# Kernel optimization log

Hardware: AMD Instinct MI355X
Metric: run time of the kernel (lower is better)

## Reference

```python
import jax, jax.numpy as jnp
import numpy as np

N = 100000       # patches per slide (bag size)
D = 512          # size[1] for size_arg='big'
D_ATTN = 256     # size[2]
C = 4            # n_classes
N_REFS = 3
TP_RATE = 0.01
NP_RATE = 0.01
REF_RATE = 0.01
EPS = 1e-10


def setup_inputs() -> dict:
    key = jax.random.key(0)
    ks = jax.random.split(key, 8)
    w = lambda k, shape: jax.random.normal(k, shape, jnp.float32) * 0.02
    return {
        "h": jax.random.normal(ks[0], (N, D), jnp.float32),
        "label": jax.random.randint(ks[1], (2,), 0, C),
        "Wa": w(ks[2], (D, D_ATTN)), "ba": jnp.zeros((D_ATTN,), jnp.float32),
        "Wb": w(ks[3], (D, D_ATTN)), "bb": jnp.zeros((D_ATTN,), jnp.float32),
        "Wc": w(ks[4], (D_ATTN, C)), "bc": jnp.zeros((C,), jnp.float32),
        "Wcls": w(ks[5], (D, C)), "bcls": jnp.zeros((C,), jnp.float32),
        "Wr": w(ks[6], (N_REFS, D, C + 1)),
        "br": jnp.zeros((N_REFS, C + 1), jnp.float32),
    }


def _ce(logits, targets):
    # cross entropy with integer targets, reduction='none'
    logp = jax.nn.log_softmax(logits, axis=-1)
    return -jnp.take_along_axis(logp, targets[..., None], axis=-1)[..., 0]


def _find_candidate_loss(final_score, h, in_label, Wr, br):
    n = final_score.shape[0]
    k = max(1, int(n * TP_RATE))
    mn = final_score.min(axis=0)
    mx = final_score.max(axis=0)
    norm = (final_score - mn) / (mx - mn)                     # [N, C]
    vals, idx = jax.lax.top_k(norm.T, k)                      # [C, k]
    valid = (vals > 0.5) & in_label[:, None]                  # only classes in label
    logits = jnp.einsum('ckd,de->cke', h[idx], Wr) + br       # [C, k, C+1]
    tgt = jnp.broadcast_to(jnp.arange(C)[:, None], (C, k))
    ce_tp = _ce(logits, tgt)
    mean_score = final_score.mean(axis=1)
    k_np = int(n * NP_RATE)
    nvals, nidx = jax.lax.top_k(-mean_score, k_np)
    np_valid = (-nvals) < 0.5
    np_logits = h[nidx] @ Wr + br                             # [k_np, C+1]
    ce_np = -jax.nn.log_softmax(np_logits, axis=-1)[:, C]
    num = jnp.sum(ce_tp * valid) + jnp.sum(ce_np * np_valid)
    den = valid.sum() + np_valid.sum()
    return num / jnp.maximum(den, 1)


def _find_candidate_ref_loss(ref_score, h, in_label, Wr, br):
    n = ref_score.shape[0]
    k = max(1, int(n * REF_RATE))
    vals, idx = jax.lax.top_k(ref_score.T, k)                 # [C+1, k]
    include = jnp.concatenate([in_label, jnp.array([True])])  # bg class always included
    valid = (vals > 0.5) & include[:, None]
    logits = jnp.einsum('ckd,de->cke', h[idx], Wr) + br       # [C+1, k, C+1]
    tgt = jnp.broadcast_to(jnp.arange(C + 1)[:, None], (C + 1, k))
    ce = _ce(logits, tgt)
    return jnp.sum(ce * valid) / jnp.maximum(valid.sum(), 1)


def _forward(h, label, Wa, ba, Wb, bb, Wc, bc, Wcls, bcls, Wr, br):
    # gated attention (Attn_Net_Gated), eval mode (dropout off)
    a = jnp.tanh(h @ Wa + ba)
    b = jax.nn.sigmoid(h @ Wb + bb)
    det_logit = (a * b) @ Wc + bc                             # [N, C]
    cls_score = jax.nn.softmax(h @ Wcls + bcls, axis=1)
    det_score = jax.nn.softmax(det_logit, axis=0)             # softmax over instances
    final_score = cls_score * det_score
    in_label = jnp.any(jnp.arange(C)[:, None] == label[None, :], axis=1)  # [C] bool
    instance_loss = jnp.float32(0.0)
    ref_score = final_score
    for r in range(N_REFS):
        if r == 0:
            instance_loss = instance_loss + _find_candidate_loss(final_score, h, in_label, Wr[r], br[r])
        else:
            instance_loss = instance_loss + _find_candidate_ref_loss(ref_score, h, in_label, Wr[r], br[r])
        ref_score = jax.nn.softmax(h @ Wr[r] + br[r], axis=1)  # [N, C+1]
    Y_prob = jnp.clip(jnp.sum(final_score, axis=0), EPS, 1.0 - EPS)
    return final_score, Y_prob, ref_score, instance_loss


def reference(h, label, Wa, ba, Wb, bb, Wc, bc, Wcls, bcls, Wr, br):
    final_score, Y_prob, ref_score, instance_loss = _forward(
        h, label, Wa, ba, Wb, bb, Wc, bc, Wcls, bcls, Wr, br)
    Y_hat = jnp.argmax(Y_prob)[None]
    return final_score, Y_prob, Y_hat, ref_score, instance_loss
```

## Files before the change

kernel.cpp:

```cpp
#include <hip/hip_runtime.h>
#include <math.h>

#define NI    100000
#define KSEL  1000
#define NCOL2 640
#define HBINS 2048

#define OUT_FS   0
#define OUT_YP   400000
#define OUT_YH   400004
#define OUT_REF  400005
#define OUT_LOSS 900005

#define OFF_DET    0
#define OFF_CLS    400000
#define OFF_REF0   800000
#define OFF_REF1   1300000
#define OFF_MEAN   1800000
#define OFF_WPT    1900000
#define OFF_BPACK  2063840
#define OFF_SCAL   2064480
#define OFF_SELIDX 2064608
#define OFF_HIST   2079608

#define SC_SUMEXP 0
#define SC_YPROB  4
#define SC_FSMIN  8
#define SC_FSMAX  12
#define SC_THR    16
#define SC_INCL   20
#define SC_NUM    25
#define SC_CNT    28
#define SC_PREFIX 43
#define SC_RESTK  58

typedef short short8 __attribute__((ext_vector_type(8)));
typedef float f32x4 __attribute__((ext_vector_type(4)));

__device__ __forceinline__ unsigned fenc(float x) {
    unsigned u = __float_as_uint(x);
    return (u & 0x80000000u) ? ~u : (u | 0x80000000u);
}
__device__ __forceinline__ unsigned short f2bf(float f) {
    unsigned u = __float_as_uint(f);
    return (unsigned short)((u + 0x7FFFu + ((u >> 16) & 1u)) >> 16);
}

__global__ __launch_bounds__(256) void prep_kernel(
    const float* __restrict__ Wa, const float* __restrict__ Wb,
    const float* __restrict__ Wcls, const float* __restrict__ Wr,
    const float* __restrict__ ba, const float* __restrict__ bb,
    const float* __restrict__ bcls, const float* __restrict__ br,
    float* __restrict__ ws)
{
    const int tid0 = blockIdx.x * 256 + threadIdx.x;
    unsigned short* wpT = (unsigned short*)(ws + OFF_WPT);
    if (tid0 < NCOL2 * 512) {
        const int c = tid0 >> 9, k = tid0 & 511;
        float v = 0.f;
        if (c < 512)      { const int j = c >> 1; v = (c & 1) ? Wb[k*256 + j] : Wa[k*256 + j]; }
        else if (c < 516)   v = Wcls[k*4 + (c - 512)];
        else if (c < 531) { const int q = c - 516; v = Wr[((q/5)*512 + k)*5 + (q%5)]; }
        wpT[tid0] = f2bf(v);
    }
    if (tid0 < NCOL2) {
        float v = 0.f; const int c = tid0;
        if (c < 512)      v = (c & 1) ? bb[c >> 1] : ba[c >> 1];
        else if (c < 516) v = bcls[c - 512];
        else if (c < 531) v = br[c - 516];
        ws[OFF_BPACK + c] = v;
    }
    if (tid0 < 128) {
        unsigned* su = (unsigned*)(ws + OFF_SCAL);
        unsigned v = 0u;
        if (tid0 >= SC_FSMIN && tid0 < SC_FSMIN + 4)   v = 0xFFFFFFFFu;
        if (tid0 >= SC_RESTK && tid0 < SC_RESTK + 15)  v = (unsigned)KSEL;
        su[tid0] = v;
    }
    unsigned* hist = (unsigned*)(ws + OFF_HIST);
    if (tid0 < 15 * HBINS) hist[tid0] = 0u;
}

__global__ __launch_bounds__(256, 2) void gemm_mfma(
    const float* __restrict__ h, const unsigned short* __restrict__ wpT,
    const float* __restrict__ bpack, const float* __restrict__ Wc,
    const float* __restrict__ bc,
    float* __restrict__ det_logit, float* __restrict__ det_sumexp,
    float* __restrict__ cls_score, float* __restrict__ ref0,
    float* __restrict__ ref1, float* __restrict__ out_ref2)
{
    __shared__ alignas(16) unsigned char smem[74304];
    unsigned short* Als = (unsigned short*)smem;
    float* slog  = (float*)smem;
    float* sbias = (float*)(smem + 66560);
    float* sWc   = (float*)(smem + 69120);
    float* sdet  = (float*)(smem + 73216);
    float* sred  = (float*)(smem + 74240);

    const int tid  = threadIdx.x;
    const int lane = tid & 63;
    const int w    = tid >> 6;
    const int wm   = (w >> 1) * 32;
    const int wn   = (w & 1) * 64;
    const int lrow = lane & 15, lq = lane >> 4;
    const int row_base = blockIdx.x * 64;

    for (int t = tid; t < 640;  t += 256) sbias[t] = bpack[t];
    for (int t = tid; t < 1024; t += 256) sWc[t]   = Wc[t];
    if (tid < 64) { sdet[tid*4+0] = 0.f; sdet[tid*4+1] = 0.f; sdet[tid*4+2] = 0.f; sdet[tid*4+3] = 0.f; }

    #pragma unroll
    for (int pass = 0; pass < 4; ++pass) {
        float4 tmp[8];
        #pragma unroll
        for (int it = 0; it < 8; ++it) {
            const int q = (pass*8 + it)*256 + tid;
            const int r = q >> 7, c4 = q & 127;
            const int grow = row_base + r;
            tmp[it] = (grow < NI) ? *(const float4*)&h[(size_t)grow * 512 + c4*4]
                                  : make_float4(0.f, 0.f, 0.f, 0.f);
        }
        #pragma unroll
        for (int it = 0; it < 8; ++it) {
            const int q = (pass*8 + it)*256 + tid;
            const int r = q >> 7, c4 = q & 127;
            ushort4 pk;
            pk.x = f2bf(tmp[it].x); pk.y = f2bf(tmp[it].y);
            pk.z = f2bf(tmp[it].z); pk.w = f2bf(tmp[it].w);
            *(ushort4*)&Als[r*520 + c4*4] = pk;
        }
    }
    __syncthreads();

    for (int cb = 0; cb < 5; ++cb) {
        const int n0 = cb * 128;
        const unsigned short* bp0 = wpT + (size_t)(n0 + wn + lrow) * 512 + lq*8;

        f32x4 acc[2][4];
        #pragma unroll
        for (int mt = 0; mt < 2; ++mt)
            #pragma unroll
            for (int nt = 0; nt < 4; ++nt) acc[mt][nt] = (f32x4)0.f;

        uint4 bnext[4];
        #pragma unroll
        for (int nt = 0; nt < 4; ++nt) bnext[nt] = *(const uint4*)(bp0 + nt*16*512);

        for (int kc = 0; kc < 512; kc += 32) {
            uint4 bcur[4];
            #pragma unroll
            for (int nt = 0; nt < 4; ++nt) bcur[nt] = bnext[nt];
            if (kc + 32 < 512) {
                #pragma unroll
                for (int nt = 0; nt < 4; ++nt)
                    bnext[nt] = *(const uint4*)(bp0 + nt*16*512 + kc + 32);
            }
            short8 af[2];
            #pragma unroll
            for (int mt = 0; mt < 2; ++mt)
                af[mt] = *(const short8*)&Als[(wm + mt*16 + lrow)*520 + kc + lq*8];
            #pragma unroll
            for (int mt = 0; mt < 2; ++mt)
                #pragma unroll
                for (int nt = 0; nt < 4; ++nt)
                    acc[mt][nt] = __builtin_amdgcn_mfma_f32_16x16x32_bf16(
                        af[mt], *(const short8*)&bcur[nt], acc[mt][nt], 0, 0, 0);
        }

        if (cb < 4) {
            #pragma unroll
            for (int mt = 0; mt < 2; ++mt) {
                #pragma unroll
                for (int reg = 0; reg < 4; ++reg) {
                    float c0 = 0.f, c1 = 0.f, c2 = 0.f, c3 = 0.f;
                    #pragma unroll
                    for (int nt = 0; nt < 4; ++nt) {
                        const int cl = wn + nt*16 + lrow;
                        const float v = acc[mt][nt][reg] + sbias[n0 + cl];
                        const float p = __shfl_xor(v, 1);
                        const float ve = (lane & 1) ? p : v;
                        const float vo = (lane & 1) ? v : p;
                        const float e2 = __expf(2.f * ve);
                        const float gate = (1.f - 2.f / (e2 + 1.f)) * (1.f / (1.f + __expf(-vo)));
                        if (!(lane & 1)) {
                            const int j = (n0 + cl) >> 1;
                            c0 += gate * sWc[j*4+0]; c1 += gate * sWc[j*4+1];
                            c2 += gate * sWc[j*4+2]; c3 += gate * sWc[j*4+3];
                        }
                    }
                    #pragma unroll
                    for (int m = 1; m <= 8; m <<= 1) {
                        c0 += __shfl_xor(c0, m); c1 += __shfl_xor(c1, m);
                        c2 += __shfl_xor(c2, m); c3 += __shfl_xor(c3, m);
                    }
                    if ((lane & 15) == 0) {
                        const int rl = wm + mt*16 + lq*4 + reg;
                        atomicAdd(&sdet[rl*4+0], c0); atomicAdd(&sdet[rl*4+1], c1);
                        atomicAdd(&sdet[rl*4+2], c2); atomicAdd(&sdet[rl*4+3], c3);
                    }
                }
            }
        } else {
            __syncthreads();
            if (wn == 0) {
                #pragma unroll
                for (int mt = 0; mt < 2; ++mt)
                    #pragma unroll
                    for (int reg = 0; reg < 4; ++reg)
                        #pragma unroll
                        for (int nt = 0; nt < 2; ++nt) {
                            const int cl = nt*16 + lrow;
                            if (cl < 19) {
                                const int row = wm + mt*16 + lq*4 + reg;
                                slog[row * 20 + cl] = acc[mt][nt][reg] + sbias[512 + cl];
                            }
                        }
            }
            __syncthreads();
            if (tid < 64) {
                const int grow = row_base + tid;
                if (grow < NI) {
                    float L[19];
                    #pragma unroll
                    for (int q = 0; q < 19; ++q) L[q] = slog[tid * 20 + q];
                    {
                        float m = fmaxf(fmaxf(L[0], L[1]), fmaxf(L[2], L[3]));
                        float e0 = __expf(L[0]-m), e1 = __expf(L[1]-m), e2 = __expf(L[2]-m), e3 = __expf(L[3]-m);
                        const float inv = 1.f / (e0 + e1 + e2 + e3);
                        cls_score[(size_t)grow*4+0] = e0*inv; cls_score[(size_t)grow*4+1] = e1*inv;
                        cls_score[(size_t)grow*4+2] = e2*inv; cls_score[(size_t)grow*4+3] = e3*inv;
                    }
                    #pragma unroll
                    for (int r = 0; r < 3; ++r) {
                        float m = L[4+5*r];
                        #pragma unroll
                        for (int e = 1; e < 5; ++e) m = fmaxf(m, L[4+5*r+e]);
                        float ev[5]; float s = 0.f;
                        #pragma unroll
                        for (int e = 0; e < 5; ++e) { ev[e] = __expf(L[4+5*r+e] - m); s += ev[e]; }
                        const float inv = 1.f / s;
                        float* dst = (r == 0) ? ref0 : ((r == 1) ? ref1 : out_ref2);
                        #pragma unroll
                        for (int e = 0; e < 5; ++e) dst[(size_t)grow*5+e] = ev[e] * inv;
                    }
                }
            }
        }
    }
    __syncthreads();

    float e0 = 0.f, e1 = 0.f, e2 = 0.f, e3 = 0.f;
    if (tid < 64) {
        const int grow = row_base + tid;
        const float d0 = sdet[tid*4+0] + bc[0];
        const float d1 = sdet[tid*4+1] + bc[1];
        const float d2 = sdet[tid*4+2] + bc[2];
        const float d3 = sdet[tid*4+3] + bc[3];
        if (grow < NI) {
            float4 dv = make_float4(d0, d1, d2, d3);
            *(float4*)&det_logit[(size_t)grow * 4] = dv;
            e0 = __expf(d0); e1 = __expf(d1); e2 = __expf(d2); e3 = __expf(d3);
        }
    }
    #pragma unroll
    for (int m = 1; m < 64; m <<= 1) {
        e0 += __shfl_xor(e0, m); e1 += __shfl_xor(e1, m);
        e2 += __shfl_xor(e2, m); e3 += __shfl_xor(e3, m);
    }
    if (lane == 0) { sred[w*4+0] = e0; sred[w*4+1] = e1; sred[w*4+2] = e2; sred[w*4+3] = e3; }
    __syncthreads();
    if (tid < 4)
        atomicAdd(&det_sumexp[tid], sred[0+tid] + sred[4+tid] + sred[8+tid] + sred[12+tid]);
}

__global__ __launch_bounds__(256) void final_kernel(const float* __restrict__ det_logit,
        const float* __restrict__ cls_score, const float* __restrict__ det_sumexp,
        float* __restrict__ out_fs, float* __restrict__ mean_sc, float* __restrict__ yprob_sum,
        unsigned* __restrict__ fs_min_enc, unsigned* __restrict__ fs_max_enc)
{
    __shared__ float ssum[4][4], smin[4][4], smax[4][4];
    const int i = blockIdx.x * 256 + threadIdx.x;
    const bool valid = i < NI;
    float f[4]; float tot = 0.f;
    #pragma unroll
    for (int c = 0; c < 4; ++c) {
        float v = 0.f;
        if (valid) {
            const float ds = __expf(det_logit[(size_t)i*4+c]) / det_sumexp[c];
            v = cls_score[(size_t)i*4+c] * ds;
            out_fs[(size_t)i*4+c] = v;
        }
        f[c] = v; tot += v;
    }
    if (valid) mean_sc[i] = 0.25f * tot;
    float sm[4], mn[4], mx[4];
    #pragma unroll
    for (int c = 0; c < 4; ++c) {
        sm[c] = f[c];
        mn[c] = valid ? f[c] : 3.4e38f;
        mx[c] = valid ? f[c] : -3.4e38f;
    }
    #pragma unroll
    for (int c = 0; c < 4; ++c)
        #pragma unroll
        for (int m = 1; m < 64; m <<= 1) {
            sm[c] += __shfl_xor(sm[c], m, 64);
            mn[c] = fminf(mn[c], __shfl_xor(mn[c], m, 64));
            mx[c] = fmaxf(mx[c], __shfl_xor(mx[c], m, 64));
        }
    const int w = threadIdx.x >> 6;
    if ((threadIdx.x & 63) == 0) {
        #pragma unroll
        for (int c = 0; c < 4; ++c) { ssum[w][c] = sm[c]; smin[w][c] = mn[c]; smax[w][c] = mx[c]; }
    }
    __syncthreads();
    if (threadIdx.x < 4) {
        const int c = threadIdx.x;
        float S = 0.f, MN = 3.4e38f, MX = -3.4e38f;
        #pragma unroll
        for (int w2 = 0; w2 < 4; ++w2) {
            S += ssum[w2][c]; MN = fminf(MN, smin[w2][c]); MX = fmaxf(MX, smax[w2][c]);
        }
        atomicAdd(&yprob_sum[c], S);
        atomicMin(&fs_min_enc[c], fenc(MN));
        atomicMax(&fs_max_enc[c], fenc(MX));
    }
}

__global__ void scalars_kernel(const int* __restrict__ label, float* __restrict__ out,
                               float* __restrict__ ws_scal)
{
    if (blockIdx.x == 0 && threadIdx.x == 0) {
        float* sf = ws_scal; unsigned* su = (unsigned*)ws_scal; int* si = (int*)ws_scal;
        float best = -1.f; int arg = 0;
        for (int c = 0; c < 4; ++c) {
            float v = sf[SC_YPROB + c];
            v = fminf(fmaxf(v, 1e-10f), 1.f - 1e-10f);
            out[OUT_YP + c] = v;
            if (v > best) { best = v; arg = c; }
        }
        out[OUT_YH] = (float)arg;
        for (int c = 0; c < 4; ++c) {
            unsigned ue = su[SC_FSMIN + c], ux = su[SC_FSMAX + c];
            float mn = (ue & 0x80000000u) ? __uint_as_float(ue & 0x7FFFFFFFu) : __uint_as_float(~ue);
            float mx = (ux & 0x80000000u) ? __uint_as_float(ux & 0x7FFFFFFFu) : __uint_as_float(~ux);
            sf[SC_THR + c] = mn + 0.5f * (mx - mn);
        }
        const int l0 = label[0], l1 = label[1];
        for (int c = 0; c < 4; ++c) si[SC_INCL + c] = (l0 == c || l1 == c) ? 1 : 0;
        si[SC_INCL + 4] = 1;
    }
}

__device__ __forceinline__ float sel_value(int b, int i, const float* fs, const float* mean,
                                           const float* r0, const float* r1) {
    if (b < 4)  return fs[(size_t)i*4 + b];
    if (b == 4) return mean[i];
    if (b < 10) return r0[(size_t)i*5 + (b-5)];
    return r1[(size_t)i*5 + (b-10)];
}

__global__ __launch_bounds__(256) void hist_kernel(const float* __restrict__ fs,
        const float* __restrict__ mean, const float* __restrict__ r0, const float* __restrict__ r1,
        unsigned* __restrict__ hist, const float* __restrict__ ws_scal, int shift, int width)
{
    const int b = blockIdx.x;
    const unsigned* su = (const unsigned*)ws_scal;
    const int* si = (const int*)ws_scal;
    const int c = (b < 4) ? b : ((b == 4) ? -1 : ((b < 10) ? b - 5 : b - 10));
    if (c >= 0 && !si[SC_INCL + c]) return;
    __shared__ unsigned lh[HBINS];
    const int nbins = 1 << width;
    for (int t = threadIdx.x; t < nbins; t += 256) lh[t] = 0u;
    __syncthreads();
    const int pb = shift + width;
    const unsigned prefix = su[SC_PREFIX + b];
    const unsigned mask = (unsigned)(nbins - 1);
    for (int i = blockIdx.y * 256 + threadIdx.x; i < NI; i += 8 * 256) {
        const float v = sel_value(b, i, fs, mean, r0, r1);
        const unsigned u = fenc(b == 4 ? -v : v);
        if (pb >= 32 || (u >> pb) == prefix)
            atomicAdd(&lh[(u >> shift) & mask], 1u);
    }
    __syncthreads();
    for (int t = threadIdx.x; t < nbins; t += 256)
        if (lh[t]) atomicAdd(&hist[(size_t)b * HBINS + t], lh[t]);
}

__global__ __launch_bounds__(256) void scan_kernel(unsigned* __restrict__ hist,
                                                   float* __restrict__ ws_scal, int width)
{
    __shared__ unsigned csum[256];
    const int b = blockIdx.x;
    unsigned* su = (unsigned*)ws_scal;
    unsigned* hh = hist + (size_t)b * HBINS;
    const int nbins = 1 << width;
    const int chunk = (nbins + 255) >> 8;
    unsigned s = 0;
    for (int j = 0; j < chunk; ++j) {
        const int idx = threadIdx.x * chunk + j;
        if (idx < nbins) s += hh[idx];
    }
    csum[threadIdx.x] = s;
    __syncthreads();
    if (threadIdx.x == 0) {
        const unsigned K = su[SC_RESTK + b];
        unsigned running = 0; unsigned found = 0; unsigned rem = K;
        int t;
        for (t = 255; t >= 0; --t) {
            if (running + csum[t] >= K) break;
            running += csum[t];
        }
        if (t < 0) t = 0;
        for (int j = chunk - 1; j >= 0; --j) {
            const int idx = t * chunk + j;
            if (idx >= nbins) continue;
            const unsigned cc = hh[idx];
            if (running + cc >= K) { found = (unsigned)idx; rem = K - running; break; }
            running += cc;
        }
        su[SC_RESTK + b] = rem;
        su[SC_PREFIX + b] = (su[SC_PREFIX + b] << width) | found;
    }
    __syncthreads();
    for (int t2 = threadIdx.x; t2 < nbins; t2 += 256) hh[t2] = 0u;
}

__global__ __launch_bounds__(256) void collect_kernel(const float* __restrict__ fs,
        const float* __restrict__ mean, const float* __restrict__ r0, const float* __restrict__ r1,
        float* __restrict__ ws_scal, int* __restrict__ sel_idx)
{
    const int b = blockIdx.x;
    unsigned* su = (unsigned*)ws_scal; int* si = (int*)ws_scal; float* sf = ws_scal;
    const int c = (b < 4) ? b : ((b == 4) ? -1 : ((b < 10) ? b - 5 : b - 10));
    if (c >= 0 && !si[SC_INCL + c]) return;
    const unsigned kth = su[SC_PREFIX + b];
    const float extra = (b < 4) ? sf[SC_THR + b] : 0.5f;
    for (int i = blockIdx.y * 256 + threadIdx.x; i < NI; i += 8 * 256) {
        const float v = sel_value(b, i, fs, mean, r0, r1);
        const unsigned u = fenc(b == 4 ? -v : v);
        const bool cond = (b == 4) ? (v < 0.5f) : (v > extra);
        if (u >= kth && cond) {
            const int pos = atomicAdd(&si[SC_CNT + b], 1);
            if (pos < KSEL) sel_idx[b * KSEL + pos] = i;
        }
    }
}

__global__ __launch_bounds__(256) void ce_kernel(const float* __restrict__ h,
        const float* __restrict__ Wr, const float* __restrict__ br,
        const int* __restrict__ sel_idx, float* __restrict__ ws_scal)
{
    const int* si = (const int*)ws_scal;
    float* sf = ws_scal;
    const int lane = threadIdx.x & 63;
    const int wid = (blockIdx.x * blockDim.x + threadIdx.x) >> 6;
    const int nw = (gridDim.x * blockDim.x) >> 6;
    float l0a = 0.f, l1a = 0.f, l2a = 0.f;
    for (int slot = wid; slot < 15 * KSEL; slot += nw) {
        const int b = slot / KSEL;
        const int j = slot - b * KSEL;
        const int cnt = min(si[SC_CNT + b], KSEL);
        if (j >= cnt) continue;
        const int i = sel_idx[b * KSEL + j];
        const int g = (b < 5) ? 0 : ((b < 10) ? 1 : 2);
        const int tgt = (b < 4) ? b : ((b == 4) ? 4 : ((b < 10) ? (b - 5) : (b - 10)));
        const float* hr = h + (size_t)i * 512;
        const float* wr = Wr + (size_t)g * 512 * 5;
        const int d0 = lane * 8;
        const float4 va = *(const float4*)&hr[d0];
        const float4 vb = *(const float4*)&hr[d0 + 4];
        const float hv[8] = {va.x, va.y, va.z, va.w, vb.x, vb.y, vb.z, vb.w};
        float acc[5] = {0.f, 0.f, 0.f, 0.f, 0.f};
        #pragma unroll
        for (int t = 0; t < 8; ++t) {
            const float* row = wr + (size_t)(d0 + t) * 5;
            #pragma unroll
            for (int e = 0; e < 5; ++e) acc[e] += hv[t] * row[e];
        }
        #pragma unroll
        for (int e = 0; e < 5; ++e)
            #pragma unroll
            for (int m = 1; m < 64; m <<= 1) acc[e] += __shfl_xor(acc[e], m, 64);
        if (lane == 0) {
            float l[5];
            #pragma unroll
            for (int e = 0; e < 5; ++e) l[e] = acc[e] + br[g * 5 + e];
            float mx = l[0];
            #pragma unroll
            for (int e = 1; e < 5; ++e) mx = fmaxf(mx, l[e]);
            float s = 0.f;
            #pragma unroll
            for (int e = 0; e < 5; ++e) s += __expf(l[e] - mx);
            const float ce = logf(s) + mx - l[tgt];
            if (g == 0) l0a += ce; else if (g == 1) l1a += ce; else l2a += ce;
        }
    }
    if (lane == 0) {
        if (l0a != 0.f) atomicAdd(&sf[SC_NUM + 0], l0a);
        if (l1a != 0.f) atomicAdd(&sf[SC_NUM + 1], l1a);
        if (l2a != 0.f) atomicAdd(&sf[SC_NUM + 2], l2a);
    }
}

__global__ void loss_kernel(const float* __restrict__ ws_scal, float* __restrict__ out)
{
    if (blockIdx.x == 0 && threadIdx.x == 0) {
        const int* si = (const int*)ws_scal;
        float loss = 0.f;
        for (int g = 0; g < 3; ++g) {
            int den = 0;
            for (int b = g * 5; b < g * 5 + 5; ++b) den += min(si[SC_CNT + b], KSEL);
            loss += ws_scal[SC_NUM + g] / (float)(den > 1 ? den : 1);
        }
        out[OUT_LOSS] = loss;
    }
}

extern "C" void kernel_launch(void* const* d_in, const int* in_sizes, int n_in,
                              void* d_out, int out_size, void* d_ws, size_t ws_size,
                              hipStream_t stream)
{
    const float* h    = (const float*)d_in[0];
    const int*   lab  = (const int*)d_in[1];
    const float* Wa   = (const float*)d_in[2];
    const float* ba   = (const float*)d_in[3];
    const float* Wb   = (const float*)d_in[4];
    const float* bb   = (const float*)d_in[5];
    const float* Wc   = (const float*)d_in[6];
    const float* bc   = (const float*)d_in[7];
    const float* Wcls = (const float*)d_in[8];
    const float* bcls = (const float*)d_in[9];
    const float* Wr   = (const float*)d_in[10];
    const float* br   = (const float*)d_in[11];
    float* out = (float*)d_out;
    float* ws  = (float*)d_ws;

    float* det_logit = ws + OFF_DET;
    float* cls_score = ws + OFF_CLS;
    float* ref0      = ws + OFF_REF0;
    float* ref1      = ws + OFF_REF1;
    float* mean_sc   = ws + OFF_MEAN;
    unsigned short* wpT = (unsigned short*)(ws + OFF_WPT);
    float* scal = ws + OFF_SCAL;
    int*   sel_idx = (int*)(ws + OFF_SELIDX);
    unsigned* hist = (unsigned*)(ws + OFF_HIST);

    hipLaunchKernelGGL(prep_kernel, dim3(1280), dim3(256), 0, stream,
                       Wa, Wb, Wcls, Wr, ba, bb, bcls, br, ws);
    hipLaunchKernelGGL(gemm_mfma, dim3(1563), dim3(256), 0, stream,
                       h, wpT, ws + OFF_BPACK, Wc, bc,
                       det_logit, scal + SC_SUMEXP, cls_score, ref0, ref1, out + OUT_REF);
    hipLaunchKernelGGL(final_kernel, dim3(391), dim3(256), 0, stream,
                       det_logit, cls_score, scal + SC_SUMEXP,
                       out + OUT_FS, mean_sc, scal + SC_YPROB,
                       (unsigned*)(scal) + SC_FSMIN, (unsigned*)(scal) + SC_FSMAX);
    hipLaunchKernelGGL(scalars_kernel, dim3(1), dim3(64), 0, stream, lab, out, scal);
    hipLaunchKernelGGL(hist_kernel, dim3(15, 8), dim3(256), 0, stream,
                       out + OUT_FS, mean_sc, ref0, ref1, hist, scal, 21, 11);
    hipLaunchKernelGGL(scan_kernel, dim3(15), dim3(256), 0, stream, hist, scal, 11);
    hipLaunchKernelGGL(hist_kernel, dim3(15, 8), dim3(256), 0, stream,
                       out + OUT_FS, mean_sc, ref0, ref1, hist, scal, 10, 11);
    hipLaunchKernelGGL(scan_kernel, dim3(15), dim3(256), 0, stream, hist, scal, 11);
    hipLaunchKernelGGL(hist_kernel, dim3(15, 8), dim3(256), 0, stream,
                       out + OUT_FS, mean_sc, ref0, ref1, hist, scal, 0, 10);
    hipLaunchKernelGGL(scan_kernel, dim3(15), dim3(256), 0, stream, hist, scal, 10);
    hipLaunchKernelGGL(collect_kernel, dim3(15, 8), dim3(256), 0, stream,
                       out + OUT_FS, mean_sc, ref0, ref1, scal, sel_idx);
    hipLaunchKernelGGL(ce_kernel, dim3(240), dim3(256), 0, stream, h, Wr, br, sel_idx, scal);
    hipLaunchKernelGGL(loss_kernel, dim3(1), dim3(64), 0, stream, scal, out);
}
```

Measured before the change: 748.2 us.

## Use eight-wave GEMM blocks with swizzled LDS and deeper B prefetch

The fused projection GEMM now runs 512 threads per block, with each of eight waves computing a 32x32 sub-tile instead of four waves computing 32x64. The bf16 copy of h in LDS moves from a padded row layout to an XOR-swizzled 1024-byte-row layout to avoid bank conflicts. B fragments are prefetched three k-steps ahead in a fully unrolled loop. The det_sumexp reduction is simplified to a single wave issuing global atomics. The aim is more latency hiding and fewer LDS conflicts. The launch bound of 512 threads with 4 blocks may cap registers tightly and cause spills.

```diff
diff --git a/kernel.cpp b/kernel.cpp
--- a/kernel.cpp
+++ b/kernel.cpp
@@ -81,7 +81,7 @@
     if (tid0 < 15 * HBINS) hist[tid0] = 0u;
 }
 
-__global__ __launch_bounds__(256, 2) void gemm_mfma(
+__global__ __launch_bounds__(512, 4) void gemm_mfma(
     const float* __restrict__ h, const unsigned short* __restrict__ wpT,
     const float* __restrict__ bpack, const float* __restrict__ Wc,
     const float* __restrict__ bc,
@@ -89,32 +89,30 @@
     float* __restrict__ cls_score, float* __restrict__ ref0,
     float* __restrict__ ref1, float* __restrict__ out_ref2)
 {
-    __shared__ alignas(16) unsigned char smem[74304];
-    unsigned short* Als = (unsigned short*)smem;
+    __shared__ alignas(16) unsigned char smem[73216];
     float* slog  = (float*)smem;
-    float* sbias = (float*)(smem + 66560);
-    float* sWc   = (float*)(smem + 69120);
-    float* sdet  = (float*)(smem + 73216);
-    float* sred  = (float*)(smem + 74240);
+    float* sbias = (float*)(smem + 65536);
+    float* sWc   = (float*)(smem + 68096);
+    float* sdet  = (float*)(smem + 72192);
 
     const int tid  = threadIdx.x;
     const int lane = tid & 63;
     const int w    = tid >> 6;
-    const int wm   = (w >> 1) * 32;
-    const int wn   = (w & 1) * 64;
+    const int wm   = (w >> 2) * 32;
+    const int wn   = (w & 3) * 32;
     const int lrow = lane & 15, lq = lane >> 4;
     const int row_base = blockIdx.x * 64;
 
-    for (int t = tid; t < 640;  t += 256) sbias[t] = bpack[t];
-    for (int t = tid; t < 1024; t += 256) sWc[t]   = Wc[t];
+    for (int t = tid; t < 640;  t += 512) sbias[t] = bpack[t];
+    for (int t = tid; t < 1024; t += 512) sWc[t]   = Wc[t];
     if (tid < 64) { sdet[tid*4+0] = 0.f; sdet[tid*4+1] = 0.f; sdet[tid*4+2] = 0.f; sdet[tid*4+3] = 0.f; }
 
     #pragma unroll
-    for (int pass = 0; pass < 4; ++pass) {
+    for (int pass = 0; pass < 2; ++pass) {
         float4 tmp[8];
         #pragma unroll
         for (int it = 0; it < 8; ++it) {
-            const int q = (pass*8 + it)*256 + tid;
+            const int q = (pass*8 + it)*512 + tid;
             const int r = q >> 7, c4 = q & 127;
             const int grow = row_base + r;
             tmp[it] = (grow < NI) ? *(const float4*)&h[(size_t)grow * 512 + c4*4]
@@ -122,49 +120,54 @@
         }
         #pragma unroll
         for (int it = 0; it < 8; ++it) {
-            const int q = (pass*8 + it)*256 + tid;
+            const int q = (pass*8 + it)*512 + tid;
             const int r = q >> 7, c4 = q & 127;
+            const int s = (c4 >> 1) ^ (r & 7);
             ushort4 pk;
             pk.x = f2bf(tmp[it].x); pk.y = f2bf(tmp[it].y);
             pk.z = f2bf(tmp[it].z); pk.w = f2bf(tmp[it].w);
-            *(ushort4*)&Als[r*520 + c4*4] = pk;
-        }
-    }
-    __syncthreads();
+            *(ushort4*)(smem + r*1024 + (s<<4) + ((c4&1)<<3)) = pk;
+        }
+    }
+    __syncthreads();
+
+    const int row0 = wm + lrow;
+    const int r7   = row0 & 7;
+    const unsigned abase = (unsigned)(row0*1024 + ((lq ^ (r7 & 3)) << 4));
+    const unsigned x64   = (unsigned)((r7 & 4) << 4);
 
     for (int cb = 0; cb < 5; ++cb) {
         const int n0 = cb * 128;
         const unsigned short* bp0 = wpT + (size_t)(n0 + wn + lrow) * 512 + lq*8;
-
-        f32x4 acc[2][4];
+        const unsigned short* bp1 = bp0 + 16*512;
+
+        f32x4 acc[2][2];
         #pragma unroll
         for (int mt = 0; mt < 2; ++mt)
             #pragma unroll
-            for (int nt = 0; nt < 4; ++nt) acc[mt][nt] = (f32x4)0.f;
-
-        uint4 bnext[4];
-        #pragma unroll
-        for (int nt = 0; nt < 4; ++nt) bnext[nt] = *(const uint4*)(bp0 + nt*16*512);
-
-        for (int kc = 0; kc < 512; kc += 32) {
-            uint4 bcur[4];
-            #pragma unroll
-            for (int nt = 0; nt < 4; ++nt) bcur[nt] = bnext[nt];
-            if (kc + 32 < 512) {
-                #pragma unroll
-                for (int nt = 0; nt < 4; ++nt)
-                    bnext[nt] = *(const uint4*)(bp0 + nt*16*512 + kc + 32);
+            for (int nt = 0; nt < 2; ++nt) acc[mt][nt] = (f32x4)0.f;
+
+        uint4 bb0[3], bb1[3];
+        bb0[0] = *(const uint4*)(bp0);      bb1[0] = *(const uint4*)(bp1);
+        bb0[1] = *(const uint4*)(bp0+32);   bb1[1] = *(const uint4*)(bp1+32);
+        bb0[2] = *(const uint4*)(bp0+64);   bb1[2] = *(const uint4*)(bp1+64);
+
+        #pragma unroll
+        for (int s = 0; s < 16; ++s) {
+            const int kc = s * 32;
+            const uint4 b0 = bb0[s % 3];
+            const uint4 b1 = bb1[s % 3];
+            if (s + 3 < 16) {
+                bb0[s % 3] = *(const uint4*)(bp0 + kc + 96);
+                bb1[s % 3] = *(const uint4*)(bp1 + kc + 96);
             }
-            short8 af[2];
-            #pragma unroll
-            for (int mt = 0; mt < 2; ++mt)
-                af[mt] = *(const short8*)&Als[(wm + mt*16 + lrow)*520 + kc + lq*8];
-            #pragma unroll
-            for (int mt = 0; mt < 2; ++mt)
-                #pragma unroll
-                for (int nt = 0; nt < 4; ++nt)
-                    acc[mt][nt] = __builtin_amdgcn_mfma_f32_16x16x32_bf16(
-                        af[mt], *(const short8*)&bcur[nt], acc[mt][nt], 0, 0, 0);
+            const unsigned aoff = abase + (((unsigned)(kc*2)) ^ x64);
+            const short8 af0 = *(const short8*)(smem + aoff);
+            const short8 af1 = *(const short8*)(smem + aoff + 16384);
+            acc[0][0] = __builtin_amdgcn_mfma_f32_16x16x32_bf16(af0, *(const short8*)&b0, acc[0][0], 0, 0, 0);
+            acc[0][1] = __builtin_amdgcn_mfma_f32_16x16x32_bf16(af0, *(const short8*)&b1, acc[0][1], 0, 0, 0);
+            acc[1][0] = __builtin_amdgcn_mfma_f32_16x16x32_bf16(af1, *(const short8*)&b0, acc[1][0], 0, 0, 0);
+            acc[1][1] = __builtin_amdgcn_mfma_f32_16x16x32_bf16(af1, *(const short8*)&b1, acc[1][1], 0, 0, 0);
         }
 
         if (cb < 4) {
@@ -174,7 +177,7 @@
                 for (int reg = 0; reg < 4; ++reg) {
                     float c0 = 0.f, c1 = 0.f, c2 = 0.f, c3 = 0.f;
                     #pragma unroll
-                    for (int nt = 0; nt < 4; ++nt) {
+                    for (int nt = 0; nt < 2; ++nt) {
                         const int cl = wn + nt*16 + lrow;
                         const float v = acc[mt][nt][reg] + sbias[n0 + cl];
                         const float p = __shfl_xor(v, 1);
@@ -202,7 +205,7 @@
             }
         } else {
             __syncthreads();
-            if (wn == 0) {
+            if ((w & 3) == 0) {
                 #pragma unroll
                 for (int mt = 0; mt < 2; ++mt)
                     #pragma unroll
@@ -249,9 +252,9 @@
     }
     __syncthreads();
 
-    float e0 = 0.f, e1 = 0.f, e2 = 0.f, e3 = 0.f;
-    if (tid < 64) {
+    if (w == 0) {
         const int grow = row_base + tid;
+        float e0 = 0.f, e1 = 0.f, e2 = 0.f, e3 = 0.f;
         const float d0 = sdet[tid*4+0] + bc[0];
         const float d1 = sdet[tid*4+1] + bc[1];
         const float d2 = sdet[tid*4+2] + bc[2];
@@ -261,16 +264,16 @@
             *(float4*)&det_logit[(size_t)grow * 4] = dv;
             e0 = __expf(d0); e1 = __expf(d1); e2 = __expf(d2); e3 = __expf(d3);
         }
-    }
-    #pragma unroll
-    for (int m = 1; m < 64; m <<= 1) {
-        e0 += __shfl_xor(e0, m); e1 += __shfl_xor(e1, m);
-        e2 += __shfl_xor(e2, m); e3 += __shfl_xor(e3, m);
-    }
-    if (lane == 0) { sred[w*4+0] = e0; sred[w*4+1] = e1; sred[w*4+2] = e2; sred[w*4+3] = e3; }
-    __syncthreads();
-    if (tid < 4)
-        atomicAdd(&det_sumexp[tid], sred[0+tid] + sred[4+tid] + sred[8+tid] + sred[12+tid]);
+        #pragma unroll
+        for (int m = 1; m < 64; m <<= 1) {
+            e0 += __shfl_xor(e0, m); e1 += __shfl_xor(e1, m);
+            e2 += __shfl_xor(e2, m); e3 += __shfl_xor(e3, m);
+        }
+        if (lane == 0) {
+            atomicAdd(&det_sumexp[0], e0); atomicAdd(&det_sumexp[1], e1);
+            atomicAdd(&det_sumexp[2], e2); atomicAdd(&det_sumexp[3], e3);
+        }
+    }
 }
 
 __global__ __launch_bounds__(256) void final_kernel(const float* __restrict__ det_logit,
@@ -548,7 +551,7 @@
 
     hipLaunchKernelGGL(prep_kernel, dim3(1280), dim3(256), 0, stream,
                        Wa, Wb, Wcls, Wr, ba, bb, bcls, br, ws);
-    hipLaunchKernelGGL(gemm_mfma, dim3(1563), dim3(256), 0, stream,
+    hipLaunchKernelGGL(gemm_mfma, dim3(1563), dim3(512), 0, stream,
                        h, wpT, ws + OFF_BPACK, Wc, bc,
                        det_logit, scal + SC_SUMEXP, cls_score, ref0, ref1, out + OUT_REF);
     hipLaunchKernelGGL(final_kernel, dim3(391), dim3(256), 0, stream,
```

Measured after the change: 737.6 us. Within noise of the previous version (-1.4%).

## Double M-tile to 128 rows, stage B via direct-to-LDS loads with swizzled A

Applied to the files above, without the earlier changes.

Each gemm block now covers 128 rows instead of 64, so every B-weight fetch feeds twice as many MFMAs. B tiles are double-buffered in LDS using global_load_lds direct loads, replacing per-wave register prefetch from global. The A tile moves to an XOR-swizzled layout to avoid bank conflicts. The cost is about 156KB of LDS, one block per CU, a barrier every k-step, and per-wave atomics for the exp-sum.

```diff
diff --git a/kernel.cpp b/kernel.cpp
--- a/kernel.cpp
+++ b/kernel.cpp
@@ -45,6 +45,11 @@
     unsigned u = __float_as_uint(f);
     return (unsigned short)((u + 0x7FFFu + ((u >> 16) & 1u)) >> 16);
 }
+__device__ __forceinline__ void gld_lds16(const void* g, void* l) {
+    __builtin_amdgcn_global_load_lds(
+        (const __attribute__((address_space(1))) unsigned int*)g,
+        (__attribute__((address_space(3))) unsigned int*)l, 16, 0, 0);
+}
 
 __global__ __launch_bounds__(256) void prep_kernel(
     const float* __restrict__ Wa, const float* __restrict__ Wb,
@@ -81,7 +86,7 @@
     if (tid0 < 15 * HBINS) hist[tid0] = 0u;
 }
 
-__global__ __launch_bounds__(256, 2) void gemm_mfma(
+__global__ __launch_bounds__(256, 1) void gemm_mfma(
     const float* __restrict__ h, const unsigned short* __restrict__ wpT,
     const float* __restrict__ bpack, const float* __restrict__ Wc,
     const float* __restrict__ bc,
@@ -89,28 +94,35 @@
     float* __restrict__ cls_score, float* __restrict__ ref0,
     float* __restrict__ ref1, float* __restrict__ out_ref2)
 {
-    __shared__ alignas(16) unsigned char smem[74304];
-    unsigned short* Als = (unsigned short*)smem;
-    float* slog  = (float*)smem;
-    float* sbias = (float*)(smem + 66560);
-    float* sWc   = (float*)(smem + 69120);
-    float* sdet  = (float*)(smem + 73216);
-    float* sred  = (float*)(smem + 74240);
+    __shared__ alignas(16) unsigned char smem[156160];
+    float* slog  = (float*)(smem + 131072);
+    float* sbias = (float*)(smem + 147456);
+    float* sWc   = (float*)(smem + 150016);
+    float* sdet  = (float*)(smem + 154112);
 
     const int tid  = threadIdx.x;
     const int lane = tid & 63;
     const int w    = tid >> 6;
-    const int wm   = (w >> 1) * 32;
+    const int wm   = (w >> 1) * 64;
     const int wn   = (w & 1) * 64;
     const int lrow = lane & 15, lq = lane >> 4;
-    const int row_base = blockIdx.x * 64;
+    const int row_base = blockIdx.x * 128;
+
+    #define STAGE_B(bufi, n0_, kc_) {                                                   \
+        const unsigned short* gs0 = wpT + (size_t)((n0_) + lane) * 512 + (kc_) + w*8;   \
+        unsigned char* lb = smem + 131072 + (bufi)*8192 + w*2048;                       \
+        gld_lds16(gs0, lb);                                                             \
+        gld_lds16(gs0 + 64*512, lb + 1024);                                             \
+    }
+
+    STAGE_B(0, 0, 0);
 
     for (int t = tid; t < 640;  t += 256) sbias[t] = bpack[t];
     for (int t = tid; t < 1024; t += 256) sWc[t]   = Wc[t];
-    if (tid < 64) { sdet[tid*4+0] = 0.f; sdet[tid*4+1] = 0.f; sdet[tid*4+2] = 0.f; sdet[tid*4+3] = 0.f; }
+    if (tid < 128) { sdet[tid*4+0] = 0.f; sdet[tid*4+1] = 0.f; sdet[tid*4+2] = 0.f; sdet[tid*4+3] = 0.f; }
 
     #pragma unroll
-    for (int pass = 0; pass < 4; ++pass) {
+    for (int pass = 0; pass < 8; ++pass) {
         float4 tmp[8];
         #pragma unroll
         for (int it = 0; it < 8; ++it) {
@@ -124,52 +136,57 @@
         for (int it = 0; it < 8; ++it) {
             const int q = (pass*8 + it)*256 + tid;
             const int r = q >> 7, c4 = q & 127;
+            const int s = (c4 >> 1) ^ (r & 7);
             ushort4 pk;
             pk.x = f2bf(tmp[it].x); pk.y = f2bf(tmp[it].y);
             pk.z = f2bf(tmp[it].z); pk.w = f2bf(tmp[it].w);
-            *(ushort4*)&Als[r*520 + c4*4] = pk;
-        }
-    }
-    __syncthreads();
-
+            *(ushort4*)(smem + r*1024 + (s<<4) + ((c4&1)<<3)) = pk;
+        }
+    }
+    __syncthreads();
+
+    const int row0 = wm + lrow;
+    const int r7   = row0 & 7;
+    const unsigned abase = (unsigned)(row0*1024 + ((lq ^ (r7 & 3)) << 4));
+    const unsigned x64   = (unsigned)((r7 & 4) << 4);
+
+    int buf = 0;
     for (int cb = 0; cb < 5; ++cb) {
         const int n0 = cb * 128;
-        const unsigned short* bp0 = wpT + (size_t)(n0 + wn + lrow) * 512 + lq*8;
-
-        f32x4 acc[2][4];
-        #pragma unroll
-        for (int mt = 0; mt < 2; ++mt)
+        f32x4 acc[4][4];
+        #pragma unroll
+        for (int mt = 0; mt < 4; ++mt)
             #pragma unroll
             for (int nt = 0; nt < 4; ++nt) acc[mt][nt] = (f32x4)0.f;
 
-        uint4 bnext[4];
-        #pragma unroll
-        for (int nt = 0; nt < 4; ++nt) bnext[nt] = *(const uint4*)(bp0 + nt*16*512);
-
-        for (int kc = 0; kc < 512; kc += 32) {
-            uint4 bcur[4];
-            #pragma unroll
-            for (int nt = 0; nt < 4; ++nt) bcur[nt] = bnext[nt];
-            if (kc + 32 < 512) {
-                #pragma unroll
-                for (int nt = 0; nt < 4; ++nt)
-                    bnext[nt] = *(const uint4*)(bp0 + nt*16*512 + kc + 32);
+        for (int s = 0; s < 16; ++s) {
+            if (!(cb == 4 && s == 15)) {
+                const int ncb = (s == 15) ? cb + 1 : cb;
+                const int nkc = (s == 15) ? 0 : (s + 1) * 32;
+                STAGE_B(buf ^ 1, ncb * 128, nkc);
             }
-            short8 af[2];
-            #pragma unroll
-            for (int mt = 0; mt < 2; ++mt)
-                af[mt] = *(const short8*)&Als[(wm + mt*16 + lrow)*520 + kc + lq*8];
-            #pragma unroll
-            for (int mt = 0; mt < 2; ++mt)
+            const unsigned aoff = abase + (((unsigned)(s * 64)) ^ x64);
+            short8 af[4], bfr[4];
+            #pragma unroll
+            for (int mt = 0; mt < 4; ++mt)
+                af[mt] = *(const short8*)(smem + aoff + mt*16384);
+            #pragma unroll
+            for (int nt = 0; nt < 4; ++nt)
+                bfr[nt] = *(const short8*)(smem + 131072 + buf*8192 + lq*2048
+                                           + (wn + nt*16 + lrow)*16);
+            #pragma unroll
+            for (int mt = 0; mt < 4; ++mt)
                 #pragma unroll
                 for (int nt = 0; nt < 4; ++nt)
                     acc[mt][nt] = __builtin_amdgcn_mfma_f32_16x16x32_bf16(
-                        af[mt], *(const short8*)&bcur[nt], acc[mt][nt], 0, 0, 0);
+                        af[mt], bfr[nt], acc[mt][nt], 0, 0, 0);
+            __syncthreads();
+            buf ^= 1;
         }
 
         if (cb < 4) {
             #pragma unroll
-            for (int mt = 0; mt < 2; ++mt) {
+            for (int mt = 0; mt < 4; ++mt) {
                 #pragma unroll
                 for (int reg = 0; reg < 4; ++reg) {
                     float c0 = 0.f, c1 = 0.f, c2 = 0.f, c3 = 0.f;
@@ -201,10 +218,9 @@
                 }
             }
         } else {
-            __syncthreads();
-            if (wn == 0) {
+            if ((w & 1) == 0) {
                 #pragma unroll
-                for (int mt = 0; mt < 2; ++mt)
+                for (int mt = 0; mt < 4; ++mt)
                     #pragma unroll
                     for (int reg = 0; reg < 4; ++reg)
                         #pragma unroll
@@ -217,7 +233,7 @@
                         }
             }
             __syncthreads();
-            if (tid < 64) {
+            if (tid < 128) {
                 const int grow = row_base + tid;
                 if (grow < NI) {
                     float L[19];
@@ -249,9 +265,9 @@
     }
     __syncthreads();
 
-    float e0 = 0.f, e1 = 0.f, e2 = 0.f, e3 = 0.f;
-    if (tid < 64) {
+    if (tid < 128) {
         const int grow = row_base + tid;
+        float e0 = 0.f, e1 = 0.f, e2 = 0.f, e3 = 0.f;
         const float d0 = sdet[tid*4+0] + bc[0];
         const float d1 = sdet[tid*4+1] + bc[1];
         const float d2 = sdet[tid*4+2] + bc[2];
@@ -261,16 +277,17 @@
             *(float4*)&det_logit[(size_t)grow * 4] = dv;
             e0 = __expf(d0); e1 = __expf(d1); e2 = __expf(d2); e3 = __expf(d3);
         }
-    }
-    #pragma unroll
-    for (int m = 1; m < 64; m <<= 1) {
-        e0 += __shfl_xor(e0, m); e1 += __shfl_xor(e1, m);
-        e2 += __shfl_xor(e2, m); e3 += __shfl_xor(e3, m);
-    }
-    if (lane == 0) { sred[w*4+0] = e0; sred[w*4+1] = e1; sred[w*4+2] = e2; sred[w*4+3] = e3; }
-    __syncthreads();
-    if (tid < 4)
-        atomicAdd(&det_sumexp[tid], sred[0+tid] + sred[4+tid] + sred[8+tid] + sred[12+tid]);
+        #pragma unroll
+        for (int m = 1; m < 64; m <<= 1) {
+            e0 += __shfl_xor(e0, m); e1 += __shfl_xor(e1, m);
+            e2 += __shfl_xor(e2, m); e3 += __shfl_xor(e3, m);
+        }
+        if (lane == 0) {
+            atomicAdd(&det_sumexp[0], e0); atomicAdd(&det_sumexp[1], e1);
+            atomicAdd(&det_sumexp[2], e2); atomicAdd(&det_sumexp[3], e3);
+        }
+    }
+    #undef STAGE_B
 }
 
 __global__ __launch_bounds__(256) void final_kernel(const float* __restrict__ det_logit,
@@ -548,7 +565,7 @@
 
     hipLaunchKernelGGL(prep_kernel, dim3(1280), dim3(256), 0, stream,
                        Wa, Wb, Wcls, Wr, ba, bb, bcls, br, ws);
-    hipLaunchKernelGGL(gemm_mfma, dim3(1563), dim3(256), 0, stream,
+    hipLaunchKernelGGL(gemm_mfma, dim3(782), dim3(256), 0, stream,
                        h, wpT, ws + OFF_BPACK, Wc, bc,
                        det_logit, scal + SC_SUMEXP, cls_score, ref0, ref1, out + OUT_REF);
     hipLaunchKernelGGL(final_kernel, dim3(391), dim3(256), 0, stream,
```

After: 880.7 us. 1.18x slower.
